# Performance work log

Measured on AMD Instinct MI355X. Metric: run time of the kernel, lower is better.

Reference implementation:

```python
import jax, jax.numpy as jnp
import numpy as np

HIDDEN = 1024
FFN = 2048
NUM_EXPERTS = 16
JITTER_EPS = 0.01


def setup_inputs() -> dict:
    key = jax.random.key(0)
    k1, k2, k3, k4 = jax.random.split(key, 4)
    hidden_states = jax.random.normal(k1, (4, 2048, HIDDEN), dtype=jnp.float32)
    gate_weight = jax.random.normal(k2, (NUM_EXPERTS, HIDDEN), dtype=jnp.float32) * 0.02
    # gate_up_weights[e, :FFN] = w1 (gate proj), [FFN:] = w3 (up proj)
    gate_up_weights = jax.random.normal(k3, (NUM_EXPERTS, 2 * FFN, HIDDEN), dtype=jnp.float32) * 0.02
    down_weights = jax.random.normal(k4, (NUM_EXPERTS, HIDDEN, FFN), dtype=jnp.float32) * 0.02
    return {
        'hidden_states': hidden_states,
        'gate_weight': gate_weight,
        'gate_up_weights': gate_up_weights,
        'down_weights': down_weights,
    }


def sparsemixer(scores, jitter_eps):
    # top-1 selection with jitter mask
    m1 = jnp.max(scores, axis=-1, keepdims=True)              # [T,1]
    ind1 = jnp.argmax(scores, axis=-1, keepdims=True)         # [T,1]
    factor1 = jnp.maximum(jnp.abs(scores), m1)
    mask1 = (m1 - scores) / factor1 > 2.0 * jitter_eps
    gates1 = jax.nn.softmax(jnp.where(mask1, -jnp.inf, scores), axis=-1)
    w1 = jnp.take_along_axis(gates1, ind1, axis=-1)           # [T,1]

    # mask out top-1, select top-2
    top1_onehot = jax.nn.one_hot(ind1[:, 0], scores.shape[-1], dtype=bool)
    masked_scores = jnp.where(top1_onehot, -jnp.inf, scores)
    m2 = jnp.max(masked_scores, axis=-1, keepdims=True)
    ind2 = jnp.argmax(masked_scores, axis=-1, keepdims=True)
    factor2 = jnp.maximum(jnp.abs(scores), m2)
    mask2 = (m2 - scores) / factor2 > 2.0 * jitter_eps
    gates2 = jax.nn.softmax(jnp.where(mask2, -jnp.inf, masked_scores), axis=-1)
    w2 = jnp.take_along_axis(gates2, ind2, axis=-1)           # [T,1]

    multipliers = jnp.concatenate([w1, w2], axis=-1)          # [T,2]
    experts = jnp.concatenate([ind1, ind2], axis=-1)          # [T,2] int
    return multipliers, experts


def fused_moe(x, gate_up_weights, down_weights, routing_weights, selected_experts):
    # x: [T,H], gate_up: [E,2F,H], down: [E,H,F]
    E = gate_up_weights.shape[0]
    ffn = down_weights.shape[2]
    # combine[t,e] = sum_k routing_weights[t,k] * (selected[t,k]==e)
    onehot = jax.nn.one_hot(selected_experts, E, dtype=x.dtype)     # [T,2,E]
    combine = jnp.einsum('tk,tke->te', routing_weights, onehot)     # [T,E]
    out = jnp.zeros_like(x)
    for e in range(E):
        gu = x @ gate_up_weights[e].T                                # [T,2F]
        h = jax.nn.silu(gu[:, :ffn]) * gu[:, ffn:]                   # [T,F]
        out = out + combine[:, e:e + 1] * (h @ down_weights[e].T)    # [T,H]
    return out


def reference(hidden_states, gate_weight, gate_up_weights, down_weights):
    B, S, H = hidden_states.shape
    x = hidden_states.reshape(-1, H)                         # [T,H]
    router_logits = x @ gate_weight.T                        # [T,E]
    routing_weights, selected_experts = sparsemixer(router_logits, JITTER_EPS)
    out = fused_moe(x, gate_up_weights, down_weights, routing_weights, selected_experts)
    return out.reshape(B, S, H), router_logits
```

## Files before the change

### kernel.cpp

```cpp
#include <hip/hip_runtime.h>
#include <hip/hip_bf16.h>
#include <math.h>

#define T_TOKENS 8192
#define HID 1024
#define FFN 2048
#define NEXP 16
#define NPAIR (2*T_TOKENS)
#define TM 128
#define MAXTILES 144

typedef short bf16x8 __attribute__((ext_vector_type(8)));
typedef float f32x4 __attribute__((ext_vector_type(4)));

static const size_t HPACK_OFF = 0;
static const size_t HPACK_SZ  = (size_t)MAXTILES * 32 * 16384;
static const size_t GPACK_OFF = HPACK_OFF + HPACK_SZ;
static const size_t GPACK_SZ  = (size_t)16 * 64 * 16 * 8192;
static const size_t DPACK_OFF = GPACK_OFF + GPACK_SZ;
static const size_t DPACK_SZ  = (size_t)16 * 16 * 32 * 8192;
static const size_t APACK_OFF = DPACK_OFF + DPACK_SZ;
static const size_t APACK_SZ  = (size_t)MAXTILES * 16 * 16384;
static const size_t WTK_OFF   = APACK_OFF + APACK_SZ;
static const size_t ETK_OFF   = WTK_OFF  + (size_t)NPAIR*4;
static const size_t RANK_OFF  = ETK_OFF  + (size_t)NPAIR*4;
static const size_t LIST_OFF  = RANK_OFF + (size_t)NPAIR*4;
static const size_t CNT_OFF   = LIST_OFF + (size_t)NPAIR*4;
static const size_t OFFS_OFF  = CNT_OFF  + 64;
static const size_t TEXP_OFF  = OFFS_OFF + 128;
static const size_t TSEG_OFF  = TEXP_OFF + (size_t)MAXTILES*4;
static const size_t HDR_OFF   = TSEG_OFF + (size_t)MAXTILES*4;

__device__ __forceinline__ unsigned short f2bf(float f) {
  union { float f; unsigned u; } v; v.f = f;
  unsigned r = v.u + 0x7fff + ((v.u >> 16) & 1);
  return (unsigned short)(r >> 16);
}

__device__ __forceinline__ float bf2f(unsigned short u) {
  union { unsigned u; float f; } v; v.u = ((unsigned)u) << 16; return v.f;
}

__device__ __forceinline__ bf16x8 pack8(float4 a, float4 b) {
  bf16x8 r;
  r[0]=(short)f2bf(a.x); r[1]=(short)f2bf(a.y); r[2]=(short)f2bf(a.z); r[3]=(short)f2bf(a.w);
  r[4]=(short)f2bf(b.x); r[5]=(short)f2bf(b.y); r[6]=(short)f2bf(b.z); r[7]=(short)f2bf(b.w);
  return r;
}

__device__ __forceinline__ void ld16(const unsigned short* g, unsigned short* l) {
  __builtin_amdgcn_global_load_lds((const __attribute__((address_space(1))) void*)g,
                                   (__attribute__((address_space(3))) void*)l, 16, 0, 0);
}

#define WAITV4 do { asm volatile("s_waitcnt vmcnt(4)" ::: "memory"); } while (0)
#define WAITV0 do { asm volatile("s_waitcnt vmcnt(0)" ::: "memory"); } while (0)
#define WAITL0 do { asm volatile("s_waitcnt lgkmcnt(0)" ::: "memory"); __builtin_amdgcn_sched_barrier(0); } while (0)
#define XBAR   do { __builtin_amdgcn_s_barrier(); __builtin_amdgcn_sched_barrier(0); } while (0)

__device__ __forceinline__ void pack_body(const float* __restrict__ src, unsigned short* __restrict__ dst,
                                          int e, int nb, int kb, int nbcnt, int kbcnt, int kdim,
                                          unsigned short* tile ) {
  int tid = threadIdx.x;
  int n = tid >> 2, ks = (tid & 3) * 16;
  const float* s = src + ((size_t)((e*nbcnt + nb)*64 + n))*kdim + kb*64 + ks;
  float4 f0 = *(const float4*)(s);
  float4 f1 = *(const float4*)(s + 4);
  float4 f2 = *(const float4*)(s + 8);
  float4 f3 = *(const float4*)(s + 12);
  int kkc0 = ks >> 3;
  *(bf16x8*)&tile[(kkc0*64 + n)*8]     = pack8(f0, f1);
  *(bf16x8*)&tile[((kkc0+1)*64 + n)*8] = pack8(f2, f3);
  __syncthreads();
  unsigned short* d = dst + ((size_t)(e*nbcnt + nb)*kbcnt + kb)*4096 + tid*16;
  *(bf16x8*)(d)     = *(const bf16x8*)&tile[tid*16];
  *(bf16x8*)(d + 8) = *(const bf16x8*)&tile[tid*16 + 8];
}

__global__ __launch_bounds__(256) void k_pre(const float* __restrict__ gup,
                                             unsigned short* __restrict__ gpack,
                                             const float* __restrict__ x,
                                             const float* __restrict__ gw,
                                             float* __restrict__ logits) {
  __shared__ __align__(16) unsigned short tile[4096];
  int bid = blockIdx.x;
  if (bid < 16384) {
    int kb = bid & 15, nb = (bid >> 4) & 63, e = bid >> 10;
    pack_body(gup, gpack, e, nb, kb, 64, 16, HID, tile);
    return;
  }
  int lb = bid - 16384;
  int tid = threadIdx.x;
  int wave = tid >> 6, lane = tid & 63;
  int t = lb * 4 + wave;
  const float* xp = x + (size_t)t * HID;
  float acc[NEXP];
  #pragma unroll
  for (int e = 0; e < NEXP; e++) acc[e] = 0.f;
  #pragma unroll
  for (int it = 0; it < 4; ++it) {
    int i = it*256 + lane*4;
    float4 xv = *(const float4*)(xp + i);
    #pragma unroll
    for (int e = 0; e < NEXP; e++) {
      float4 g = *(const float4*)(gw + e*HID + i);
      acc[e] += xv.x*g.x + xv.y*g.y + xv.z*g.z + xv.w*g.w;
    }
  }
  float mine = 0.f;
  #pragma unroll
  for (int e = 0; e < NEXP; e++) {
    float v = acc[e];
    #pragma unroll
    for (int o = 32; o > 0; o >>= 1) v += __shfl_xor(v, o, 64);
    if (lane == e) mine = v;
  }
  if (lane < NEXP) logits[(size_t)t*NEXP + lane] = mine;
}

__global__ __launch_bounds__(256) void k_route(const float* __restrict__ logits,
                                               float* __restrict__ wtk, int* __restrict__ etk,
                                               int* __restrict__ rank, int* __restrict__ counts) {
  __shared__ int lcnt[NEXP];
  __shared__ int lbase[NEXP];
  int tid = threadIdx.x;
  int t = blockIdx.x*256 + tid;
  if (tid < NEXP) lcnt[tid] = 0;
  __syncthreads();

  float s[NEXP];
  const float* lp = logits + (size_t)t*NEXP;
  #pragma unroll
  for (int e = 0; e < NEXP; e++) s[e] = lp[e];

  float m1 = s[0]; int i1 = 0;
  #pragma unroll
  for (int e = 1; e < NEXP; e++) if (s[e] > m1) { m1 = s[e]; i1 = e; }
  float sum1 = 0.f;
  #pragma unroll
  for (int e = 0; e < NEXP; e++) {
    float f = fmaxf(fabsf(s[e]), m1);
    if (!((m1 - s[e]) > 0.02f*f)) sum1 += expf(s[e]-m1);
  }
  float m2 = -INFINITY; int i2 = 0;
  #pragma unroll
  for (int e = 0; e < NEXP; e++) if (e != i1 && s[e] > m2) { m2 = s[e]; i2 = e; }
  float sum2 = 0.f;
  #pragma unroll
  for (int e = 0; e < NEXP; e++) {
    if (e == i1) continue;
    float f = fmaxf(fabsf(s[e]), m2);
    if (!((m2 - s[e]) > 0.02f*f)) sum2 += expf(s[e]-m2);
  }
  wtk[t*2]   = 1.f/sum1;
  wtk[t*2+1] = 1.f/sum2;
  etk[t*2]   = i1;
  etk[t*2+1] = i2;
  int r1 = atomicAdd(&lcnt[i1], 1);
  int r2 = atomicAdd(&lcnt[i2], 1);
  __syncthreads();
  if (tid < NEXP) lbase[tid] = atomicAdd(&counts[tid], lcnt[tid]);
  __syncthreads();
  rank[t*2]   = lbase[i1] + r1;
  rank[t*2+1] = lbase[i2] + r2;
}

__global__ void k_scan(const int* __restrict__ counts, int* __restrict__ offsets,
                       int* __restrict__ texp, int* __restrict__ tseg, int* __restrict__ hdr) {
  if (threadIdx.x != 0 || blockIdx.x != 0) return;
  int off = 0, nt = 0;
  for (int e = 0; e < NEXP; e++) {
    offsets[e] = off;
    int c = counts[e];
    int tiles = (c + TM - 1)/TM;
    for (int i = 0; i < tiles; i++) { texp[nt] = e; tseg[nt] = i; nt++; }
    off += c;
  }
  offsets[NEXP] = off;
  hdr[0] = nt;
}

__global__ __launch_bounds__(256) void k_scatter(const int* __restrict__ etk,
                                                 const int* __restrict__ rank,
                                                 const int* __restrict__ offsets,
                                                 int* __restrict__ list) {
  int p = blockIdx.x*256 + threadIdx.x;
  if (p >= NPAIR) return;
  int e = etk[p];
  list[offsets[e] + rank[p]] = p;
}

__global__ __launch_bounds__(256) void k_agather(const float* __restrict__ x,
                                                 const int* __restrict__ list,
                                                 const int* __restrict__ counts,
                                                 const int* __restrict__ offsets,
                                                 const int* __restrict__ texp,
                                                 const int* __restrict__ tseg,
                                                 const int* __restrict__ hdr,
                                                 unsigned short* __restrict__ apack) {
  int by = blockIdx.x;
  if (by >= hdr[0]) return;
  int e = texp[by];
  int m0 = tseg[by]*TM;
  int seg0 = offsets[e];
  int cnt = counts[e];
  __shared__ int toks[TM];
  int tid = threadIdx.x;
  if (tid < TM) toks[tid] = list[seg0 + min(m0 + tid, cnt-1)] >> 1;
  __syncthreads();
  #pragma unroll 4
  for (int it = 0; it < 64; ++it) {
    int flat = it*256 + tid;
    int kb = flat >> 10;
    int i  = flat & 1023;
    int kkc = i >> 7, row = i & 127;
    const float* s = x + (size_t)toks[row]*HID + kb*64 + kkc*8;
    float4 f0 = *(const float4*)(s);
    float4 f1 = *(const float4*)(s + 4);
    *(bf16x8*)(apack + ((size_t)(by*16 + kb))*8192 + (size_t)i*8) = pack8(f0, f1);
  }
}

__global__ __launch_bounds__(256,4) void k_gateup(const unsigned short* __restrict__ apack,
                                                  const unsigned short* __restrict__ gpack,
                                                  const float* __restrict__ dwn,
                                                  unsigned short* __restrict__ dpack,
                                                  const float* __restrict__ wtk,
                                                  const int* __restrict__ list,
                                                  const int* __restrict__ counts,
                                                  const int* __restrict__ offsets,
                                                  const int* __restrict__ texp,
                                                  const int* __restrict__ tseg,
                                                  const int* __restrict__ hdr,
                                                  unsigned short* __restrict__ hpack) {
  __shared__ __align__(16) unsigned short A_lds[2][4096];
  __shared__ __align__(16) unsigned short Bg_lds[2][2048];
  __shared__ __align__(16) unsigned short Bu_lds[2][2048];
  int bid = blockIdx.x;
  if (bid >= 4608) {
    int p = bid - 4608;
    pack_body(dwn, dpack, p >> 9, (p >> 5) & 15, p & 31, 16, 32, FFN, &A_lds[0][0]);
    return;
  }
  int fb = bid & 31;
  int by = bid >> 5;
  if (by >= hdr[0]) return;
  int e = texp[by];
  int m0 = tseg[by]*TM;
  int seg0 = offsets[e];
  int cnt = counts[e];
  int rows = min(TM, cnt - m0);

  int tid = threadIdx.x;
  int wid = tid >> 6, lane = tid & 63;
  int wr = wid >> 1, wc = wid & 1;
  int c4 = lane >> 4, r16 = lane & 15;

  const unsigned short* gA = apack + (size_t)by * 131072;
  const unsigned short* gG = gpack + ((size_t)(e*64 + fb))      * 65536;
  const unsigned short* gU = gpack + ((size_t)(e*64 + 32 + fb)) * 65536;

  f32x4 accg[4][2] = {};
  f32x4 accu[4][2] = {};

  auto STAGE = [&](int buf, int kb) {
    #pragma unroll
    for (int s = 0; s < 4; ++s) {
      int i = wid*4 + s;
      if (i < 8) {
        ld16(gA + (size_t)kb*4096 + i*512 + lane*8, &A_lds[buf][i*512]);
      } else if (i < 12) {
        int j = i - 8;
        ld16(gG + (size_t)kb*2048 + j*512 + lane*8, &Bg_lds[buf][j*512]);
      } else {
        int j = i - 12;
        ld16(gU + (size_t)kb*2048 + j*512 + lane*8, &Bu_lds[buf][j*512]);
      }
    }
  };

  auto COMPUTE = [&](int buf) {
    bf16x8 a[4], bg[2], bu[2];
    #pragma unroll
    for (int sm = 0; sm < 4; ++sm)
      a[sm] = *(const bf16x8*)&A_lds[buf][(c4*128 + wr*64 + sm*16 + r16)*8];
    #pragma unroll
    for (int sn = 0; sn < 2; ++sn) {
      bg[sn] = *(const bf16x8*)&Bg_lds[buf][(c4*64 + wc*32 + sn*16 + r16)*8];
      bu[sn] = *(const bf16x8*)&Bu_lds[buf][(c4*64 + wc*32 + sn*16 + r16)*8];
    }
    #pragma unroll
    for (int sm = 0; sm < 4; ++sm)
      #pragma unroll
      for (int sn = 0; sn < 2; ++sn) {
        accg[sm][sn] = __builtin_amdgcn_mfma_f32_16x16x32_bf16(a[sm], bg[sn], accg[sm][sn], 0, 0, 0);
        accu[sm][sn] = __builtin_amdgcn_mfma_f32_16x16x32_bf16(a[sm], bu[sn], accu[sm][sn], 0, 0, 0);
      }
  };

  STAGE(0, 0);
  STAGE(1, 1);
  int cur = 0;
  for (int kb = 0; kb < 31; ++kb) {
    WAITV4; XBAR;
    COMPUTE(cur);
    WAITL0; XBAR;
    if (kb < 30) STAGE(cur, kb + 2);
    cur ^= 1;
  }
  WAITV0; XBAR;
  COMPUTE(cur);
  __syncthreads();

  unsigned short* scr = &A_lds[0][0];
  #pragma unroll
  for (int sm = 0; sm < 4; ++sm) {
    #pragma unroll
    for (int j = 0; j < 4; ++j) {
      int row = wr*64 + sm*16 + (lane>>4)*4 + j;
      float w = (row < rows) ? wtk[list[seg0 + m0 + row]] : 0.f;
      #pragma unroll
      for (int sn = 0; sn < 2; ++sn) {
        int col = wc*32 + sn*16 + (lane & 15);
        float g = accg[sm][sn][j];
        float u = accu[sm][sn][j];
        float hv = g / (1.f + __expf(-g)) * u * w;
        scr[((col>>3)*128 + row)*8 + (col&7)] = f2bf(hv);
      }
    }
  }
  __syncthreads();
  unsigned short* dst = hpack + ((size_t)(by*32 + fb))*8192 + tid*32;
  const unsigned short* srcl = scr + tid*32;
  #pragma unroll
  for (int q = 0; q < 4; ++q)
    *(bf16x8*)(dst + q*8) = *(const bf16x8*)(srcl + q*8);
}

__global__ __launch_bounds__(256,4) void k_down(const unsigned short* __restrict__ hpack,
                                                const unsigned short* __restrict__ dpack,
                                                const int* __restrict__ counts,
                                                const int* __restrict__ texp,
                                                const int* __restrict__ tseg,
                                                const int* __restrict__ offsets,
                                                const int* __restrict__ hdr,
                                                unsigned short* __restrict__ ydown) {
  int nb = blockIdx.x;
  int by = blockIdx.y;
  if (by >= hdr[0]) return;
  int e = texp[by];
  int m0 = tseg[by]*TM;
  int seg0 = offsets[e];
  int cnt = counts[e];
  int rows = min(TM, cnt - m0);

  __shared__ __align__(16) unsigned short A_lds[2][4096];
  __shared__ __align__(16) unsigned short B_lds[2][4096];

  int tid = threadIdx.x;
  int wid = tid >> 6, lane = tid & 63;
  int wr = wid >> 1, wc = wid & 1;
  int c4 = lane >> 4, r16 = lane & 15;

  const unsigned short* hA = hpack + (size_t)by * 262144;

  f32x4 acc[4][4] = {};

  auto STAGE = [&](int buf, int kb) {
    #pragma unroll
    for (int s = 0; s < 4; ++s) {
      int i = wid*4 + s;
      if (i < 8) {
        ld16(hA + (size_t)kb*4096 + i*512 + lane*8, &A_lds[buf][i*512]);
      } else {
        int i2 = i - 8;
        int p = i2 >> 2, j = i2 & 3;
        ld16(dpack + (((size_t)(e*16 + nb*2 + p))*32 + (kb>>1))*4096 + (kb&1)*2048 + j*512 + lane*8,
             &B_lds[buf][p*2048 + j*512]);
      }
    }
  };

  auto COMPUTE = [&](int buf) {
    bf16x8 a[4], b[4];
    #pragma unroll
    for (int sm = 0; sm < 4; ++sm)
      a[sm] = *(const bf16x8*)&A_lds[buf][(c4*128 + wr*64 + sm*16 + r16)*8];
    #pragma unroll
    for (int sn = 0; sn < 4; ++sn) {
      int col = wc*64 + sn*16 + r16;
      b[sn] = *(const bf16x8*)&B_lds[buf][(col>>6)*2048 + (c4*64 + (col&63))*8];
    }
    #pragma unroll
    for (int sm = 0; sm < 4; ++sm)
      #pragma unroll
      for (int sn = 0; sn < 4; ++sn)
        acc[sm][sn] = __builtin_amdgcn_mfma_f32_16x16x32_bf16(a[sm], b[sn], acc[sm][sn], 0, 0, 0);
  };

  STAGE(0, 0);
  STAGE(1, 1);
  int cur = 0;
  for (int kb = 0; kb < 63; ++kb) {
    WAITV4; XBAR;
    COMPUTE(cur);
    WAITL0; XBAR;
    if (kb < 62) STAGE(cur, kb + 2);
    cur ^= 1;
  }
  WAITV0; XBAR;
  COMPUTE(cur);

  #pragma unroll
  for (int sm = 0; sm < 4; ++sm) {
    #pragma unroll
    for (int j = 0; j < 4; ++j) {
      int row = wr*64 + sm*16 + (lane>>4)*4 + j;
      if (row < rows) {
        size_t slot = (size_t)(seg0 + m0 + row);
        #pragma unroll
        for (int sn = 0; sn < 4; ++sn) {
          int col = nb*128 + wc*64 + sn*16 + r16;
          ydown[slot*HID + col] = f2bf(acc[sm][sn][j]);
        }
      }
    }
  }
}

__global__ __launch_bounds__(256) void k_final(const unsigned short* __restrict__ ydown,
                                               const int* __restrict__ etk,
                                               const int* __restrict__ rank,
                                               const int* __restrict__ offsets,
                                               float* __restrict__ out) {
  int t = blockIdx.x;
  int c = threadIdx.x;
  int p0 = t*2, p1 = t*2 + 1;
  int s0 = offsets[etk[p0]] + rank[p0];
  int s1 = offsets[etk[p1]] + rank[p1];
  ushort4 a = *(const ushort4*)(ydown + (size_t)s0*HID + c*4);
  ushort4 b = *(const ushort4*)(ydown + (size_t)s1*HID + c*4);
  float4 r;
  r.x = bf2f(a.x) + bf2f(b.x);
  r.y = bf2f(a.y) + bf2f(b.y);
  r.z = bf2f(a.z) + bf2f(b.z);
  r.w = bf2f(a.w) + bf2f(b.w);
  *(float4*)(out + (size_t)t*HID + c*4) = r;
}

extern "C" void kernel_launch(void* const* d_in, const int* in_sizes, int n_in,
                              void* d_out, int out_size, void* d_ws, size_t ws_size,
                              hipStream_t stream) {
  const float* x   = (const float*)d_in[0];
  const float* gw  = (const float*)d_in[1];
  const float* gup = (const float*)d_in[2];
  const float* dwn = (const float*)d_in[3];

  float* out = (float*)d_out;
  float* logits = out + (size_t)T_TOKENS*HID;

  char* ws = (char*)d_ws;
  unsigned short* hpack = (unsigned short*)(ws + HPACK_OFF);
  unsigned short* gpack = (unsigned short*)(ws + GPACK_OFF);
  unsigned short* dpack = (unsigned short*)(ws + DPACK_OFF);
  unsigned short* apack = (unsigned short*)(ws + APACK_OFF);
  unsigned short* ydown = (unsigned short*)(ws + GPACK_OFF);
  float* wtk   = (float*)(ws + WTK_OFF);
  int* etk     = (int*)(ws + ETK_OFF);
  int* rank    = (int*)(ws + RANK_OFF);
  int* list    = (int*)(ws + LIST_OFF);
  int* counts  = (int*)(ws + CNT_OFF);
  int* offsets = (int*)(ws + OFFS_OFF);
  int* texp    = (int*)(ws + TEXP_OFF);
  int* tseg    = (int*)(ws + TSEG_OFF);
  int* hdr     = (int*)(ws + HDR_OFF);

  hipMemsetAsync(counts, 0, 64, stream);

  k_pre<<<16384 + 2048, 256, 0, stream>>>(gup, gpack, x, gw, logits);

  k_route<<<T_TOKENS/256, 256, 0, stream>>>(logits, wtk, etk, rank, counts);
  k_scan<<<1, 64, 0, stream>>>(counts, offsets, texp, tseg, hdr);
  k_scatter<<<NPAIR/256, 256, 0, stream>>>(etk, rank, offsets, list);
  k_agather<<<MAXTILES, 256, 0, stream>>>(x, list, counts, offsets, texp, tseg, hdr, apack);

  k_gateup<<<4608 + 8192, 256, 0, stream>>>(apack, gpack, dwn, dpack, wtk, list, counts, offsets,
                                            texp, tseg, hdr, hpack);

  dim3 g4(8, MAXTILES);
  k_down<<<g4, 256, 0, stream>>>(hpack, dpack, counts, texp, tseg, offsets, hdr, ydown);

  k_final<<<T_TOKENS, 256, 0, stream>>>(ydown, etk, rank, offsets, out);
}
```

Measured before the change: 457.0 us.

## Drop scan and final-combine kernels; inline tile map and atomically accumulate down output

Removes the single-thread scan kernel: every block now recomputes its expert, tile offset and segment base from the 16 expert counts, and scatter builds offsets in shared memory. The bf16 ydown buffer and the final combine kernel are also removed. The down GEMM now atomically adds its fp32 results straight into the zeroed output at the owning token row. This saves two launches plus a full write and read of the intermediate buffer, at the cost of a memset of the output, scattered fp32 atomics, and a summation order that is no longer deterministic.

```diff
diff --git a/kernel.cpp b/kernel.cpp
--- a/kernel.cpp
+++ b/kernel.cpp
@@ -26,19 +26,11 @@
 static const size_t RANK_OFF  = ETK_OFF  + (size_t)NPAIR*4;
 static const size_t LIST_OFF  = RANK_OFF + (size_t)NPAIR*4;
 static const size_t CNT_OFF   = LIST_OFF + (size_t)NPAIR*4;
-static const size_t OFFS_OFF  = CNT_OFF  + 64;
-static const size_t TEXP_OFF  = OFFS_OFF + 128;
-static const size_t TSEG_OFF  = TEXP_OFF + (size_t)MAXTILES*4;
-static const size_t HDR_OFF   = TSEG_OFF + (size_t)MAXTILES*4;
 
 __device__ __forceinline__ unsigned short f2bf(float f) {
   union { float f; unsigned u; } v; v.f = f;
   unsigned r = v.u + 0x7fff + ((v.u >> 16) & 1);
   return (unsigned short)(r >> 16);
-}
-
-__device__ __forceinline__ float bf2f(unsigned short u) {
-  union { unsigned u; float f; } v; v.u = ((unsigned)u) << 16; return v.f;
 }
 
 __device__ __forceinline__ bf16x8 pack8(float4 a, float4 b) {
@@ -53,6 +45,20 @@
                                    (__attribute__((address_space(3))) void*)l, 16, 0, 0);
 }
 
+__device__ __forceinline__ int tilemap(const int* __restrict__ counts, int by,
+                                       int& e, int& m0, int& seg0) {
+  int off = 0, nt = 0; e = -1; m0 = 0; seg0 = 0;
+  #pragma unroll
+  for (int ee = 0; ee < NEXP; ++ee) {
+    int c = counts[ee];
+    int tiles = (c + TM - 1) >> 7;
+    if (e < 0 && by < nt + tiles) { e = ee; m0 = (by - nt) * TM; seg0 = off; }
+    nt += tiles;
+    off += c;
+  }
+  return nt;
+}
+
 #define WAITV4 do { asm volatile("s_waitcnt vmcnt(4)" ::: "memory"); } while (0)
 #define WAITV0 do { asm volatile("s_waitcnt vmcnt(0)" ::: "memory"); } while (0)
 #define WAITL0 do { asm volatile("s_waitcnt lgkmcnt(0)" ::: "memory"); __builtin_amdgcn_sched_barrier(0); } while (0)
@@ -60,7 +66,7 @@
 
 __device__ __forceinline__ void pack_body(const float* __restrict__ src, unsigned short* __restrict__ dst,
                                           int e, int nb, int kb, int nbcnt, int kbcnt, int kdim,
-                                          unsigned short* tile ) {
+                                          unsigned short* tile) {
   int tid = threadIdx.x;
   int n = tid >> 2, ks = (tid & 3) * 16;
   const float* s = src + ((size_t)((e*nbcnt + nb)*64 + n))*kdim + kb*64 + ks;
@@ -165,44 +171,31 @@
   rank[t*2+1] = lbase[i2] + r2;
 }
 
-__global__ void k_scan(const int* __restrict__ counts, int* __restrict__ offsets,
-                       int* __restrict__ texp, int* __restrict__ tseg, int* __restrict__ hdr) {
-  if (threadIdx.x != 0 || blockIdx.x != 0) return;
-  int off = 0, nt = 0;
-  for (int e = 0; e < NEXP; e++) {
-    offsets[e] = off;
-    int c = counts[e];
-    int tiles = (c + TM - 1)/TM;
-    for (int i = 0; i < tiles; i++) { texp[nt] = e; tseg[nt] = i; nt++; }
-    off += c;
-  }
-  offsets[NEXP] = off;
-  hdr[0] = nt;
-}
-
 __global__ __launch_bounds__(256) void k_scatter(const int* __restrict__ etk,
                                                  const int* __restrict__ rank,
-                                                 const int* __restrict__ offsets,
+                                                 const int* __restrict__ counts,
                                                  int* __restrict__ list) {
-  int p = blockIdx.x*256 + threadIdx.x;
-  if (p >= NPAIR) return;
+  __shared__ int offs[NEXP];
+  int tid = threadIdx.x;
+  if (tid == 0) {
+    int off = 0;
+    #pragma unroll
+    for (int e = 0; e < NEXP; ++e) { offs[e] = off; off += counts[e]; }
+  }
+  __syncthreads();
+  int p = blockIdx.x*256 + tid;
   int e = etk[p];
-  list[offsets[e] + rank[p]] = p;
+  list[offs[e] + rank[p]] = p;
 }
 
 __global__ __launch_bounds__(256) void k_agather(const float* __restrict__ x,
                                                  const int* __restrict__ list,
                                                  const int* __restrict__ counts,
-                                                 const int* __restrict__ offsets,
-                                                 const int* __restrict__ texp,
-                                                 const int* __restrict__ tseg,
-                                                 const int* __restrict__ hdr,
                                                  unsigned short* __restrict__ apack) {
   int by = blockIdx.x;
-  if (by >= hdr[0]) return;
-  int e = texp[by];
-  int m0 = tseg[by]*TM;
-  int seg0 = offsets[e];
+  int e, m0, seg0;
+  int nt = tilemap(counts, by, e, m0, seg0);
+  if (by >= nt) return;
   int cnt = counts[e];
   __shared__ int toks[TM];
   int tid = threadIdx.x;
@@ -228,10 +221,6 @@
                                                   const float* __restrict__ wtk,
                                                   const int* __restrict__ list,
                                                   const int* __restrict__ counts,
-                                                  const int* __restrict__ offsets,
-                                                  const int* __restrict__ texp,
-                                                  const int* __restrict__ tseg,
-                                                  const int* __restrict__ hdr,
                                                   unsigned short* __restrict__ hpack) {
   __shared__ __align__(16) unsigned short A_lds[2][4096];
   __shared__ __align__(16) unsigned short Bg_lds[2][2048];
@@ -244,10 +233,9 @@
   }
   int fb = bid & 31;
   int by = bid >> 5;
-  if (by >= hdr[0]) return;
-  int e = texp[by];
-  int m0 = tseg[by]*TM;
-  int seg0 = offsets[e];
+  int e, m0, seg0;
+  int nt = tilemap(counts, by, e, m0, seg0);
+  if (by >= nt) return;
   int cnt = counts[e];
   int rows = min(TM, cnt - m0);
 
@@ -340,17 +328,13 @@
 __global__ __launch_bounds__(256,4) void k_down(const unsigned short* __restrict__ hpack,
                                                 const unsigned short* __restrict__ dpack,
                                                 const int* __restrict__ counts,
-                                                const int* __restrict__ texp,
-                                                const int* __restrict__ tseg,
-                                                const int* __restrict__ offsets,
-                                                const int* __restrict__ hdr,
-                                                unsigned short* __restrict__ ydown) {
+                                                const int* __restrict__ list,
+                                                float* __restrict__ out) {
   int nb = blockIdx.x;
   int by = blockIdx.y;
-  if (by >= hdr[0]) return;
-  int e = texp[by];
-  int m0 = tseg[by]*TM;
-  int seg0 = offsets[e];
+  int e, m0, seg0;
+  int nt = tilemap(counts, by, e, m0, seg0);
+  if (by >= nt) return;
   int cnt = counts[e];
   int rows = min(TM, cnt - m0);
 
@@ -417,35 +401,15 @@
     for (int j = 0; j < 4; ++j) {
       int row = wr*64 + sm*16 + (lane>>4)*4 + j;
       if (row < rows) {
-        size_t slot = (size_t)(seg0 + m0 + row);
+        int t = list[seg0 + m0 + row] >> 1;
         #pragma unroll
         for (int sn = 0; sn < 4; ++sn) {
           int col = nb*128 + wc*64 + sn*16 + r16;
-          ydown[slot*HID + col] = f2bf(acc[sm][sn][j]);
+          unsafeAtomicAdd(&out[(size_t)t*HID + col], acc[sm][sn][j]);
         }
       }
     }
   }
-}
-
-__global__ __launch_bounds__(256) void k_final(const unsigned short* __restrict__ ydown,
-                                               const int* __restrict__ etk,
-                                               const int* __restrict__ rank,
-                                               const int* __restrict__ offsets,
-                                               float* __restrict__ out) {
-  int t = blockIdx.x;
-  int c = threadIdx.x;
-  int p0 = t*2, p1 = t*2 + 1;
-  int s0 = offsets[etk[p0]] + rank[p0];
-  int s1 = offsets[etk[p1]] + rank[p1];
-  ushort4 a = *(const ushort4*)(ydown + (size_t)s0*HID + c*4);
-  ushort4 b = *(const ushort4*)(ydown + (size_t)s1*HID + c*4);
-  float4 r;
-  r.x = bf2f(a.x) + bf2f(b.x);
-  r.y = bf2f(a.y) + bf2f(b.y);
-  r.z = bf2f(a.z) + bf2f(b.z);
-  r.w = bf2f(a.w) + bf2f(b.w);
-  *(float4*)(out + (size_t)t*HID + c*4) = r;
 }
 
 extern "C" void kernel_launch(void* const* d_in, const int* in_sizes, int n_in,
@@ -464,31 +428,23 @@
   unsigned short* gpack = (unsigned short*)(ws + GPACK_OFF);
   unsigned short* dpack = (unsigned short*)(ws + DPACK_OFF);
   unsigned short* apack = (unsigned short*)(ws + APACK_OFF);
-  unsigned short* ydown = (unsigned short*)(ws + GPACK_OFF);
   float* wtk   = (float*)(ws + WTK_OFF);
   int* etk     = (int*)(ws + ETK_OFF);
   int* rank    = (int*)(ws + RANK_OFF);
   int* list    = (int*)(ws + LIST_OFF);
   int* counts  = (int*)(ws + CNT_OFF);
-  int* offsets = (int*)(ws + OFFS_OFF);
-  int* texp    = (int*)(ws + TEXP_OFF);
-  int* tseg    = (int*)(ws + TSEG_OFF);
-  int* hdr     = (int*)(ws + HDR_OFF);
-
+
+  hipMemsetAsync(out, 0, (size_t)T_TOKENS*HID*4, stream);
   hipMemsetAsync(counts, 0, 64, stream);
 
   k_pre<<<16384 + 2048, 256, 0, stream>>>(gup, gpack, x, gw, logits);
 
   k_route<<<T_TOKENS/256, 256, 0, stream>>>(logits, wtk, etk, rank, counts);
-  k_scan<<<1, 64, 0, stream>>>(counts, offsets, texp, tseg, hdr);
-  k_scatter<<<NPAIR/256, 256, 0, stream>>>(etk, rank, offsets, list);
-  k_agather<<<MAXTILES, 256, 0, stream>>>(x, list, counts, offsets, texp, tseg, hdr, apack);
-
-  k_gateup<<<4608 + 8192, 256, 0, stream>>>(apack, gpack, dwn, dpack, wtk, list, counts, offsets,
-                                            texp, tseg, hdr, hpack);
+  k_scatter<<<NPAIR/256, 256, 0, stream>>>(etk, rank, counts, list);
+  k_agather<<<MAXTILES, 256, 0, stream>>>(x, list, counts, apack);
+
+  k_gateup<<<4608 + 8192, 256, 0, stream>>>(apack, gpack, dwn, dpack, wtk, list, counts, hpack);
 
   dim3 g4(8, MAXTILES);
-  k_down<<<g4, 256, 0, stream>>>(hpack, dpack, counts, texp, tseg, offsets, hdr, ydown);
-
-  k_final<<<T_TOKENS, 256, 0, stream>>>(ydown, etk, rank, offsets, out);
-}
+  k_down<<<g4, 256, 0, stream>>>(hpack, dpack, counts, list, out);
+}
```

Result: no change. 463.9 us (+1.5%).
